# Kernel optimization log

Hardware: AMD Instinct MI355X
Metric: run time of the kernel (lower is better)

## Reference

```python
import jax, jax.numpy as jnp
import numpy as np


def _maxpool2x2(x):
    # x: [N, C, H, W] -> [N, C, H//2, W//2]
    return jax.lax.reduce_window(x, -jnp.inf, jax.lax.max,
                                 (1, 1, 2, 2), (1, 1, 2, 2), 'VALID')


def _head(a, W1, b1, W2, b2, W3, b3):
    # headModel: maxpool -> (adaptive avgpool to 7x7 is identity here) -> flatten -> classifier (eval mode)
    mp = _maxpool2x2(a)                      # [N, 512, 7, 7]
    flat = mp.reshape(mp.shape[0], -1)       # [N, 25088]
    h = jax.nn.relu(flat @ W1.T + b1)        # [N, 4096]
    h = jax.nn.relu(h @ W2.T + b2)           # [N, 4096]
    return h @ W3.T + b3                     # [N, 1000]


def setup_inputs() -> dict:
    key = jax.random.key(0)
    ks = jax.random.split(key, 7)
    C, HW, FC, NC = 512, 14, 4096, 1000
    acts = jax.random.uniform(ks[0], (1, C, HW, HW), dtype=jnp.float32)  # post-ReLU feature map
    s1 = 1.0 / np.sqrt(C * 7 * 7)
    s2 = 1.0 / np.sqrt(FC)
    return {
        'activations': acts,
        'W1': jax.random.normal(ks[1], (FC, C * 7 * 7), dtype=jnp.float32) * s1,
        'b1': jax.random.normal(ks[2], (FC,), dtype=jnp.float32) * 0.01,
        'W2': jax.random.normal(ks[3], (FC, FC), dtype=jnp.float32) * s2,
        'b2': jax.random.normal(ks[4], (FC,), dtype=jnp.float32) * 0.01,
        'W3': jax.random.normal(ks[5], (NC, FC), dtype=jnp.float32) * s2,
        'b3': jax.random.normal(ks[6], (NC,), dtype=jnp.float32) * 0.01,
        'ht': 224,
        'wt': 224,
    }


def reference(activations, W1, b1, W2, b2, W3, b3, ht, wt):
    C = activations.shape[1]
    logits = _head(activations, W1, b1, W2, b2, W3, b3)   # [1, 1000]
    img_class = jnp.argmax(logits[0])
    base = logits[0, img_class]

    # Batch all C channel ablations: abl[i] = activations with channel i zeroed.
    mask = (1.0 - jnp.eye(C, dtype=activations.dtype))[:, :, None, None]  # [C, C, 1, 1]
    abl = activations * mask                                              # [C, C, 14, 14]
    logits_new = _head(abl, W1, b1, W2, b2, W3, b3)                        # [C, 1000]
    alpha = (base - jnp.take(logits_new, img_class, axis=1)) / base        # [C]

    # fused = relu(sum_i alpha_i * bilinear_resize(act_i)); resize is linear,
    # so weight in activation space and do one resize (same math as the loop).
    weighted = jnp.einsum('c,chw->hw', alpha, activations[0])              # [14, 14]
    sal = jax.image.resize(weighted[None, None], (1, 1, ht, wt),
                           method='bilinear')[0, 0]                        # [ht, wt]
    fused = jax.nn.relu(sal)
    mn, mx = fused.min(), fused.max()
    denom = jnp.where(mx != mn, mx - mn, 1.0)
    fused = jnp.where(mx != mn, (fused - mn) / denom, fused)
    return fused, img_class
```

## Files before the change

### kernel.cpp

```cpp
#include <hip/hip_runtime.h>
#include <math.h>

#define CCH 512
#define F1 25088
#define FC 4096
#define NCLS 1000
#define OW 224
#define KSPLIT 8
#define KSL 512
#define PSTRIDE (CCH*FC)

#define WS_DT 0
#define WS_MP (WS_DT + FC*CCH)
#define WS_H1PRE (WS_MP + F1)
#define WS_H1 (WS_H1PRE + FC)
#define WS_H2 (WS_H1 + FC)
#define WS_H2PART (WS_H2 + FC)
#define WS_LOGITS (WS_H2PART + 8*FC)
#define WS_CLSBASE (WS_LOGITS + NCLS)
#define WS_ALPHA (WS_CLSBASE + 2)
#define WS_MINMAX (WS_ALPHA + CCH)
#define WS_LOGPART (WS_MINMAX + 2)
#define WS_A (WS_LOGPART + 64*CCH)
#define WS_PARTB (WS_A + CCH*FC/2)
#define WS_END (WS_PARTB + KSPLIT*CCH*FC/2)
#define WS_NEED_BYTES ((size_t)WS_END * 4)

typedef __attribute__((ext_vector_type(8))) short bfrag;
typedef __attribute__((ext_vector_type(4))) float f32x4;

static __device__ __forceinline__ unsigned short f2bf(float x) {
    unsigned u = __float_as_uint(x);
    unsigned r = 0x7FFFu + ((u >> 16) & 1u);
    return (unsigned short)((u + r) >> 16);
}

#define GLD16(g, l) __builtin_amdgcn_global_load_lds( \
    (const __attribute__((address_space(1))) void*)(g), \
    (__attribute__((address_space(3))) void*)(l), 16, 0, 0)

__global__ void k_maxpool(const float* __restrict__ act, float* __restrict__ ws) {
    int t = threadIdx.x;
    if (blockIdx.x == 0) {
        if (t == 0) ((int*)(ws + WS_MINMAX))[0] = 0x7F800000;
        if (t == 1) ((int*)(ws + WS_MINMAX))[1] = 0;
    }
    int idx = blockIdx.x * 256 + t;
    if (idx >= CCH * 49) return;
    int c = idx / 49, r = idx % 49, y = r / 7, x = r % 7;
    const float* a = act + c * 196 + (2 * y) * 14 + 2 * x;
    float m = fmaxf(fmaxf(a[0], a[1]), fmaxf(a[14], a[15]));
    ws[WS_MP + idx] = m;
}

__global__ __launch_bounds__(256) void k_phi7(const float* __restrict__ W1,
                                              const float* __restrict__ mp,
                                              const float* __restrict__ b1,
                                              float* __restrict__ Dt,
                                              float* __restrict__ h1pre,
                                              float* __restrict__ h1) {
    __shared__ float buf[12544];
    __shared__ float red[256];
    int j = blockIdx.x, t = threadIdx.x;
    const float4* wrow = (const float4*)(W1 + (size_t)j * F1);
    const float4* mrow = (const float4*)mp;
    float sh = 0.f;
    #pragma unroll
    for (int h = 0; h < 2; ++h) {
        const float4* src = wrow + h * 3136;
        const float4* msc = mrow + h * 3136;
        __syncthreads();
        #pragma unroll
        for (int b = 0; b < 2; ++b) {
            float4 w[6], m[6];
            #pragma unroll
            for (int e = 0; e < 6; ++e) {
                int n = t + 256 * (b * 6 + e);
                w[e] = src[n]; m[e] = msc[n];
            }
            #pragma unroll
            for (int e = 0; e < 6; ++e) {
                int n = t + 256 * (b * 6 + e);
                float4 p;
                p.x = w[e].x * m[e].x; p.y = w[e].y * m[e].y;
                p.z = w[e].z * m[e].z; p.w = w[e].w * m[e].w;
                *(float4*)&buf[n * 4] = p;
            }
        }
        if (t < 64) {
            int n = 3072 + t;
            float4 w = src[n], m = msc[n];
            float4 p;
            p.x = w.x * m.x; p.y = w.y * m.y; p.z = w.z * m.z; p.w = w.w * m.w;
            *(float4*)&buf[n * 4] = p;
        }
        __syncthreads();
        const float* bb = buf + t * 49;
        float s = 0.f;
        #pragma unroll
        for (int k = 0; k < 49; ++k) s += bb[k];
        Dt[(size_t)j * CCH + h * 256 + t] = s;
        sh += s;
    }
    red[t] = sh;
    __syncthreads();
    if (t < 128) red[t] += red[t + 128];
    __syncthreads();
    if (t < 64) {
        float v = red[t] + red[t + 64];
        for (int off = 32; off > 0; off >>= 1) v += __shfl_down(v, off, 64);
        if (t == 0) { float hv = b1[j] + v; h1pre[j] = hv; h1[j] = fmaxf(hv, 0.f); }
    }
}

template <bool RELU>
__global__ void k_gemv4096(const float* __restrict__ M, const float* __restrict__ v,
                           const float* __restrict__ bias, float* __restrict__ out) {
    int j = blockIdx.x, t = threadIdx.x;
    const float4* row = (const float4*)(M + (size_t)j * FC);
    const float4* vv = (const float4*)v;
    float s = 0.f;
    #pragma unroll
    for (int q = 0; q < 4; ++q) {
        int n = q * 256 + t;
        float4 w = row[n], x = vv[n];
        s += w.x * x.x + w.y * x.y + w.z * x.z + w.w * x.w;
    }
    __shared__ float red[256];
    red[t] = s; __syncthreads();
    if (t < 128) red[t] += red[t + 128]; __syncthreads();
    if (t < 64)  red[t] += red[t + 64];  __syncthreads();
    if (t < 64) {
        float x = red[t];
        for (int off = 32; off > 0; off >>= 1) x += __shfl_down(x, off, 64);
        if (t == 0) { float r2 = bias[j] + x; out[j] = RELU ? fmaxf(r2, 0.f) : r2; }
    }
}

__global__ void k_argmax(const float* __restrict__ logits, float* __restrict__ clsbase,
                         float* __restrict__ dout_cls) {
    int t = threadIdx.x;
    float best = -INFINITY; int bi = NCLS;
    for (int n = t; n < NCLS; n += 256) {
        float v = logits[n];
        if (v > best || (v == best && n < bi)) { best = v; bi = n; }
    }
    __shared__ float bv[256]; __shared__ int bidx[256];
    bv[t] = best; bidx[t] = bi; __syncthreads();
    for (int o = 128; o > 0; o >>= 1) {
        if (t < o) {
            float v2 = bv[t + o]; int i2 = bidx[t + o];
            if (v2 > bv[t] || (v2 == bv[t] && i2 < bidx[t])) { bv[t] = v2; bidx[t] = i2; }
        }
        __syncthreads();
    }
    if (t == 0) { clsbase[0] = (float)bidx[0]; clsbase[1] = bv[0]; *dout_cls = (float)bidx[0]; }
}

__global__ __launch_bounds__(256) void k_abuild(const float* __restrict__ Dt,
                                                const float* __restrict__ h1pre,
                                                unsigned short* __restrict__ A) {
    __shared__ unsigned short tile[64][72];
    int kt = blockIdx.x, it = blockIdx.y, t = threadIdx.x;
    int k0 = kt * 64, i0 = it * 64;
    #pragma unroll
    for (int q = 0; q < 16; ++q) {
        int kk = q * 4 + (t >> 6);
        int ii = t & 63;
        float v = fmaxf(h1pre[k0 + kk] - Dt[(size_t)(k0 + kk) * CCH + i0 + ii], 0.f);
        tile[kk][ii] = f2bf(v);
    }
    __syncthreads();
    #pragma unroll
    for (int q = 0; q < 4; ++q) {
        int c = q * 256 + t;
        int ii = c >> 4, kc = c & 15;
        ushort4 v;
        v.x = tile[kc * 4 + 0][ii]; v.y = tile[kc * 4 + 1][ii];
        v.z = tile[kc * 4 + 2][ii]; v.w = tile[kc * 4 + 3][ii];
        *(ushort4*)&A[(size_t)(i0 + ii) * FC + k0 + kc * 4] = v;
    }
}

__global__ __launch_bounds__(512) void k_mfma_v6(
    const unsigned short* __restrict__ A, const float* __restrict__ W2,
    const float* __restrict__ h1, unsigned short* __restrict__ partb,
    float* __restrict__ h2part) {
    __shared__ char As[2][32768];
    __shared__ char Bs[2][4096];
    __shared__ float h1s[KSL];
    int bid = blockIdx.x;
    int ks = bid & 7, nj = bid >> 3;
    int t = threadIdx.x;
    int wid = t >> 6, lane = t & 63, lr = lane & 15, lh = lane >> 4;
    int j0 = nj * 64;
    int kb = ks * KSL;

    h1s[t] = h1[kb + t];
    __syncthreads();

    int brow = t >> 3, bkc = t & 7;
    const float* wsrc = W2 + (size_t)(j0 + brow) * FC + kb + bkc * 4;
    int bsw = (brow & 3) ^ ((brow >> 2) & 1);
    int boff = (brow * 4 + ((bkc >> 1) ^ bsw)) * 16 + (bkc & 1) * 8;

    float hacc = 0.f;
    f32x4 acc[4][4];
    #pragma unroll
    for (int f = 0; f < 4; ++f)
        #pragma unroll
        for (int n = 0; n < 4; ++n) acc[f][n] = (f32x4){0.f, 0.f, 0.f, 0.f};

    #pragma unroll
    for (int r = 0; r < 4; ++r) {
        int c = t + 512 * r;
        int row = c >> 2, ch = c & 3;
        int sw = (row & 3) ^ ((row >> 2) & 1);
        GLD16(A + (size_t)row * FC + kb + ((ch ^ sw) * 8), As[0] + (size_t)c * 16);
    }
    {
        float4 w = *(const float4*)wsrc;
        hacc += w.x * h1s[bkc * 4 + 0] + w.y * h1s[bkc * 4 + 1]
              + w.z * h1s[bkc * 4 + 2] + w.w * h1s[bkc * 4 + 3];
        ushort4 pk;
        pk.x = f2bf(w.x); pk.y = f2bf(w.y); pk.z = f2bf(w.z); pk.w = f2bf(w.w);
        *(ushort4*)(Bs[0] + boff) = pk;
    }
    __syncthreads();

    int cur = 0;
    for (int kst = 0; kst + 32 < KSL; kst += 32) {
        int nxt = kst + 32;
        #pragma unroll
        for (int r = 0; r < 4; ++r) {
            int c = t + 512 * r;
            int row = c >> 2, ch = c & 3;
            int sw = (row & 3) ^ ((row >> 2) & 1);
            GLD16(A + (size_t)row * FC + kb + nxt + ((ch ^ sw) * 8),
                  As[cur ^ 1] + (size_t)c * 16);
        }
        float4 w = *(const float4*)(wsrc + nxt);
        {
            bfrag bfr[4];
            #pragma unroll
            for (int n = 0; n < 4; ++n) {
                int br = n * 16 + lr;
                int swb = (br & 3) ^ ((br >> 2) & 1);
                bfr[n] = *(const bfrag*)(Bs[cur] + (br * 4 + (lh ^ swb)) * 16);
            }
            #pragma unroll
            for (int f = 0; f < 4; ++f) {
                int ar = wid * 64 + f * 16 + lr;
                int swa = (ar & 3) ^ ((ar >> 2) & 1);
                bfrag av = *(const bfrag*)(As[cur] + (ar * 4 + (lh ^ swa)) * 16);
                #pragma unroll
                for (int n = 0; n < 4; ++n)
                    acc[f][n] = __builtin_amdgcn_mfma_f32_16x16x32_bf16(av, bfr[n], acc[f][n], 0, 0, 0);
            }
        }
        hacc += w.x * h1s[nxt + bkc * 4 + 0] + w.y * h1s[nxt + bkc * 4 + 1]
              + w.z * h1s[nxt + bkc * 4 + 2] + w.w * h1s[nxt + bkc * 4 + 3];
        {
            ushort4 pk;
            pk.x = f2bf(w.x); pk.y = f2bf(w.y); pk.z = f2bf(w.z); pk.w = f2bf(w.w);
            *(ushort4*)(Bs[cur ^ 1] + boff) = pk;
        }
        __syncthreads();
        cur ^= 1;
    }
    {
        bfrag bfr[4];
        #pragma unroll
        for (int n = 0; n < 4; ++n) {
            int br = n * 16 + lr;
            int swb = (br & 3) ^ ((br >> 2) & 1);
            bfr[n] = *(const bfrag*)(Bs[cur] + (br * 4 + (lh ^ swb)) * 16);
        }
        #pragma unroll
        for (int f = 0; f < 4; ++f) {
            int ar = wid * 64 + f * 16 + lr;
            int swa = (ar & 3) ^ ((ar >> 2) & 1);
            bfrag av = *(const bfrag*)(As[cur] + (ar * 4 + (lh ^ swa)) * 16);
            #pragma unroll
            for (int n = 0; n < 4; ++n)
                acc[f][n] = __builtin_amdgcn_mfma_f32_16x16x32_bf16(av, bfr[n], acc[f][n], 0, 0, 0);
        }
    }

    hacc += __shfl_down(hacc, 4, 8);
    hacc += __shfl_down(hacc, 2, 8);
    hacc += __shfl_down(hacc, 1, 8);
    if (bkc == 0) h2part[ks * FC + j0 + brow] = hacc;

    unsigned short* pb = partb + (size_t)ks * PSTRIDE;
    #pragma unroll
    for (int f = 0; f < 4; ++f) {
        int row0 = wid * 64 + f * 16 + lh * 4;
        #pragma unroll
        for (int rr = 0; rr < 4; ++rr)
            #pragma unroll
            for (int n = 0; n < 4; ++n)
                pb[(size_t)(row0 + rr) * FC + j0 + n * 16 + lr] = f2bf(acc[f][n][rr]);
    }
}

__global__ void k_h2sum(const float* __restrict__ h2part, const float* __restrict__ b2,
                        float* __restrict__ h2) {
    int j = blockIdx.x * 256 + threadIdx.x;
    if (j < FC) {
        float v = b2[j];
        #pragma unroll
        for (int p = 0; p < KSPLIT; ++p) v += h2part[p * FC + j];
        h2[j] = fmaxf(v, 0.f);
    }
}

__global__ __launch_bounds__(256) void k_alpha_b(
    const unsigned short* __restrict__ partb, const float* __restrict__ b2,
    const float* __restrict__ W3, const float* __restrict__ b3,
    const float* __restrict__ clsbase, float* __restrict__ alpha) {
    int i = blockIdx.x, t = threadIdx.x;
    int cls = (int)clsbase[0]; float base = clsbase[1];
    const float* w3r = W3 + (size_t)cls * FC;
    float s = 0.f;
    #pragma unroll
    for (int q = 0; q < 2; ++q) {
        int jj = (q * 256 + t) * 8;
        float acc8[8];
        #pragma unroll
        for (int e = 0; e < 8; ++e) acc8[e] = b2[jj + e];
        #pragma unroll
        for (int p = 0; p < KSPLIT; ++p) {
            uint4 pv = *(const uint4*)(partb + (size_t)p * PSTRIDE + (size_t)i * FC + jj);
            #pragma unroll
            for (int e = 0; e < 4; ++e) {
                unsigned a = ((const unsigned*)&pv)[e];
                acc8[e * 2]     += __uint_as_float(a << 16);
                acc8[e * 2 + 1] += __uint_as_float(a & 0xFFFF0000u);
            }
        }
        #pragma unroll
        for (int e = 0; e < 8; ++e) s += fmaxf(acc8[e], 0.f) * w3r[jj + e];
    }
    __shared__ float red[256];
    red[t] = s; __syncthreads();
    if (t < 128) red[t] += red[t + 128]; __syncthreads();
    if (t < 64)  red[t] += red[t + 64];  __syncthreads();
    if (t < 64) {
        float x = red[t];
        for (int off = 32; off > 0; off >>= 1) x += __shfl_down(x, off, 64);
        if (t == 0) alpha[i] = (base - (x + b3[cls])) / base;
    }
}

__global__ __launch_bounds__(256) void k_gemm_abl(
    const float* __restrict__ Dt, const float* __restrict__ h1pre,
    const float* __restrict__ W2, const float* __restrict__ b2,
    const float* __restrict__ W3, const float* __restrict__ clsbase,
    float* __restrict__ logit_part) {
    int mi = blockIdx.x, nj = blockIdx.y, t = threadIdx.x;
    int tx = t & 15, ty = t >> 4;
    int i0 = mi * 64, j0 = nj * 64;
    __shared__ float As2[16][64];
    __shared__ float Bs2[16][65];
    float acc[4][4] = {};
    for (int k0 = 0; k0 < FC; k0 += 16) {
        #pragma unroll
        for (int r = 0; r < 4; ++r) {
            int e = t + 256 * r; int kk = e >> 6, ii = e & 63;
            As2[kk][ii] = fmaxf(h1pre[k0 + kk] - Dt[(size_t)(k0 + kk) * CCH + i0 + ii], 0.f);
        }
        {
            int jj = t >> 2, kks = (t & 3) * 4;
            const float4 wv = *(const float4*)(W2 + (size_t)(j0 + jj) * FC + k0 + kks);
            Bs2[kks + 0][jj] = wv.x; Bs2[kks + 1][jj] = wv.y;
            Bs2[kks + 2][jj] = wv.z; Bs2[kks + 3][jj] = wv.w;
        }
        __syncthreads();
        #pragma unroll
        for (int kk = 0; kk < 16; ++kk) {
            float4 a4 = *(const float4*)&As2[kk][tx * 4];
            float av[4] = {a4.x, a4.y, a4.z, a4.w};
            float bv[4] = {Bs2[kk][ty * 4 + 0], Bs2[kk][ty * 4 + 1],
                           Bs2[kk][ty * 4 + 2], Bs2[kk][ty * 4 + 3]};
            #pragma unroll
            for (int a = 0; a < 4; ++a)
                #pragma unroll
                for (int bb = 0; bb < 4; ++bb)
                    acc[a][bb] = fmaf(av[a], bv[bb], acc[a][bb]);
        }
        __syncthreads();
    }
    int cls = (int)clsbase[0];
    const float* w3r = W3 + (size_t)cls * FC;
    float prt[4] = {0.f, 0.f, 0.f, 0.f};
    #pragma unroll
    for (int bb = 0; bb < 4; ++bb) {
        int j2 = j0 + ty * 4 + bb;
        float b2v = b2[j2], w3 = w3r[j2];
        #pragma unroll
        for (int a = 0; a < 4; ++a) prt[a] = fmaf(fmaxf(acc[a][bb] + b2v, 0.f), w3, prt[a]);
    }
    __shared__ float red2[16][68];
    #pragma unroll
    for (int a = 0; a < 4; ++a) red2[ty][tx * 4 + a] = prt[a];
    __syncthreads();
    if (t < 64) {
        float s = 0.f;
        #pragma unroll
        for (int q = 0; q < 16; ++q) s += red2[q][t];
        logit_part[nj * CCH + i0 + t] = s;
    }
}

__global__ void k_alpha_fb(const float* __restrict__ logit_part, const float* __restrict__ b3,
                           const float* __restrict__ clsbase, float* __restrict__ alpha) {
    int t = blockIdx.x * 256 + threadIdx.x;
    if (t >= CCH) return;
    int cls = (int)clsbase[0]; float base = clsbase[1];
    float s = 0.f;
    for (int q = 0; q < 64; ++q) s += logit_part[q * CCH + t];
    alpha[t] = (base - (s + b3[cls])) / base;
}

__global__ void k_resize2(const float* __restrict__ alpha, const float* __restrict__ act,
                          float* __restrict__ out, int* __restrict__ minmax) {
    __shared__ float sA[CCH];
    __shared__ float sW[196];
    int t = threadIdx.x;
    for (int i = t; i < CCH; i += 256) sA[i] = alpha[i];
    __syncthreads();
    if (t < 196) {
        float s = 0.f;
        for (int c = 0; c < CCH; ++c) s = fmaf(sA[c], act[c * 196 + t], s);
        sW[t] = s;
    }
    __syncthreads();
    int pix = blockIdx.x * 256 + t;
    int y = pix / OW, x = pix % OW;
    float uy = (y + 0.5f) * 0.0625f - 0.5f;
    float ux = (x + 0.5f) * 0.0625f - 0.5f;
    float y0f = floorf(uy), x0f = floorf(ux);
    float fy = uy - y0f, fx = ux - x0f;
    int y0 = (int)y0f, x0 = (int)x0f;
    int y0c = min(max(y0, 0), 13), y1c = min(max(y0 + 1, 0), 13);
    int x0c = min(max(x0, 0), 13), x1c = min(max(x0 + 1, 0), 13);
    float v00 = sW[y0c * 14 + x0c], v01 = sW[y0c * 14 + x1c];
    float v10 = sW[y1c * 14 + x0c], v11 = sW[y1c * 14 + x1c];
    float v0 = v00 + (v01 - v00) * fx;
    float v1 = v10 + (v11 - v10) * fx;
    float v = v0 + (v1 - v0) * fy;
    float f = fmaxf(v, 0.f);
    out[pix] = f;
    __shared__ float rmn[256], rmx[256];
    rmn[t] = f; rmx[t] = f; __syncthreads();
    for (int o = 128; o > 0; o >>= 1) {
        if (t < o) { rmn[t] = fminf(rmn[t], rmn[t + o]); rmx[t] = fmaxf(rmx[t], rmx[t + o]); }
        __syncthreads();
    }
    if (t == 0) {
        atomicMin(&minmax[0], __float_as_int(rmn[0]));
        atomicMax(&minmax[1], __float_as_int(rmx[0]));
    }
}

__global__ void k_norm(float* __restrict__ out, const int* __restrict__ minmax) {
    float mn = __int_as_float(minmax[0]);
    float mx = __int_as_float(minmax[1]);
    int pix = blockIdx.x * 256 + threadIdx.x;
    if (mx != mn) out[pix] = (out[pix] - mn) / (mx - mn);
}

extern "C" void kernel_launch(void* const* d_in, const int* in_sizes, int n_in,
                              void* d_out, int out_size, void* d_ws, size_t ws_size,
                              hipStream_t stream) {
    const float* act = (const float*)d_in[0];
    const float* W1  = (const float*)d_in[1];
    const float* b1  = (const float*)d_in[2];
    const float* W2  = (const float*)d_in[3];
    const float* b2  = (const float*)d_in[4];
    const float* W3  = (const float*)d_in[5];
    const float* b3  = (const float*)d_in[6];
    float* out = (float*)d_out;
    float* ws = (float*)d_ws;
    const bool fast = (ws_size >= WS_NEED_BYTES);

    k_maxpool<<<98, 256, 0, stream>>>(act, ws);
    k_phi7<<<4096, 256, 0, stream>>>(W1, ws + WS_MP, b1, ws + WS_DT,
                                     ws + WS_H1PRE, ws + WS_H1);
    if (fast) {
        k_abuild<<<dim3(64, 8), 256, 0, stream>>>(ws + WS_DT, ws + WS_H1PRE,
                                                  (unsigned short*)(ws + WS_A));
        k_mfma_v6<<<512, 512, 0, stream>>>(
            (const unsigned short*)(ws + WS_A), W2, ws + WS_H1,
            (unsigned short*)(ws + WS_PARTB), ws + WS_H2PART);
        k_h2sum<<<16, 256, 0, stream>>>(ws + WS_H2PART, b2, ws + WS_H2);
        k_gemv4096<false><<<1000, 256, 0, stream>>>(W3, ws + WS_H2, b3, ws + WS_LOGITS);
        k_argmax<<<1, 256, 0, stream>>>(ws + WS_LOGITS, ws + WS_CLSBASE, out + 50176);
        k_alpha_b<<<CCH, 256, 0, stream>>>((const unsigned short*)(ws + WS_PARTB), b2,
                                           W3, b3, ws + WS_CLSBASE, ws + WS_ALPHA);
    } else {
        k_gemv4096<true><<<4096, 256, 0, stream>>>(W2, ws + WS_H1, b2, ws + WS_H2);
        k_gemv4096<false><<<1000, 256, 0, stream>>>(W3, ws + WS_H2, b3, ws + WS_LOGITS);
        k_argmax<<<1, 256, 0, stream>>>(ws + WS_LOGITS, ws + WS_CLSBASE, out + 50176);
        k_gemm_abl<<<dim3(8, 64), 256, 0, stream>>>(ws + WS_DT, ws + WS_H1PRE, W2, b2,
                                                    W3, ws + WS_CLSBASE, ws + WS_LOGPART);
        k_alpha_fb<<<2, 256, 0, stream>>>(ws + WS_LOGPART, b3, ws + WS_CLSBASE,
                                          ws + WS_ALPHA);
    }
    k_resize2<<<196, 256, 0, stream>>>(ws + WS_ALPHA, act, out, (int*)(ws + WS_MINMAX));
    k_norm<<<196, 256, 0, stream>>>(out, (const int*)(ws + WS_MINMAX));
}
```

Before: 207.1 us.

## Fuse tail kernels using last-block atomic counters to cut launches

Merges the h2 sum, W3 GEMV and argmax into one kernel: every block recomputes h2 into shared memory, and the last block to finish, found with an atomic counter, does the argmax. It also merges the alpha computation, weighted sum, bilinear resize, relu and min/max normalization into a second kernel whose last block does the whole 224x224 epilogue. The aim is to remove several kernel launches and their serialization gaps. The cost is redundant h2 reduction in each of the 1000 blocks and a single-block epilogue over about 50k pixels, which runs serially on one CU.

Result: slower. 422.0 us (+103.8%).

```diff
diff --git a/kernel.cpp b/kernel.cpp
--- a/kernel.cpp
+++ b/kernel.cpp
@@ -20,7 +20,8 @@
 #define WS_CLSBASE (WS_LOGITS + NCLS)
 #define WS_ALPHA (WS_CLSBASE + 2)
 #define WS_MINMAX (WS_ALPHA + CCH)
-#define WS_LOGPART (WS_MINMAX + 2)
+#define WS_CNT (WS_MINMAX + 2)
+#define WS_LOGPART (WS_CNT + 2)
 #define WS_A (WS_LOGPART + 64*CCH)
 #define WS_PARTB (WS_A + CCH*FC/2)
 #define WS_END (WS_PARTB + KSPLIT*CCH*FC/2)
@@ -44,6 +45,8 @@
     if (blockIdx.x == 0) {
         if (t == 0) ((int*)(ws + WS_MINMAX))[0] = 0x7F800000;
         if (t == 1) ((int*)(ws + WS_MINMAX))[1] = 0;
+        if (t == 2) ((int*)(ws + WS_CNT))[0] = 0;
+        if (t == 3) ((int*)(ws + WS_CNT))[1] = 0;
     }
     int idx = blockIdx.x * 256 + t;
     if (idx >= CCH * 49) return;
@@ -111,50 +114,6 @@
         for (int off = 32; off > 0; off >>= 1) v += __shfl_down(v, off, 64);
         if (t == 0) { float hv = b1[j] + v; h1pre[j] = hv; h1[j] = fmaxf(hv, 0.f); }
     }
-}
-
-template <bool RELU>
-__global__ void k_gemv4096(const float* __restrict__ M, const float* __restrict__ v,
-                           const float* __restrict__ bias, float* __restrict__ out) {
-    int j = blockIdx.x, t = threadIdx.x;
-    const float4* row = (const float4*)(M + (size_t)j * FC);
-    const float4* vv = (const float4*)v;
-    float s = 0.f;
-    #pragma unroll
-    for (int q = 0; q < 4; ++q) {
-        int n = q * 256 + t;
-        float4 w = row[n], x = vv[n];
-        s += w.x * x.x + w.y * x.y + w.z * x.z + w.w * x.w;
-    }
-    __shared__ float red[256];
-    red[t] = s; __syncthreads();
-    if (t < 128) red[t] += red[t + 128]; __syncthreads();
-    if (t < 64)  red[t] += red[t + 64];  __syncthreads();
-    if (t < 64) {
-        float x = red[t];
-        for (int off = 32; off > 0; off >>= 1) x += __shfl_down(x, off, 64);
-        if (t == 0) { float r2 = bias[j] + x; out[j] = RELU ? fmaxf(r2, 0.f) : r2; }
-    }
-}
-
-__global__ void k_argmax(const float* __restrict__ logits, float* __restrict__ clsbase,
-                         float* __restrict__ dout_cls) {
-    int t = threadIdx.x;
-    float best = -INFINITY; int bi = NCLS;
-    for (int n = t; n < NCLS; n += 256) {
-        float v = logits[n];
-        if (v > best || (v == best && n < bi)) { best = v; bi = n; }
-    }
-    __shared__ float bv[256]; __shared__ int bidx[256];
-    bv[t] = best; bidx[t] = bi; __syncthreads();
-    for (int o = 128; o > 0; o >>= 1) {
-        if (t < o) {
-            float v2 = bv[t + o]; int i2 = bidx[t + o];
-            if (v2 > bv[t] || (v2 == bv[t] && i2 < bidx[t])) { bv[t] = v2; bidx[t] = i2; }
-        }
-        __syncthreads();
-    }
-    if (t == 0) { clsbase[0] = (float)bidx[0]; clsbase[1] = bv[0]; *dout_cls = (float)bidx[0]; }
 }
 
 __global__ __launch_bounds__(256) void k_abuild(const float* __restrict__ Dt,
@@ -304,23 +263,75 @@
     }
 }
 
-__global__ void k_h2sum(const float* __restrict__ h2part, const float* __restrict__ b2,
-                        float* __restrict__ h2) {
-    int j = blockIdx.x * 256 + threadIdx.x;
-    if (j < FC) {
-        float v = b2[j];
-        #pragma unroll
-        for (int p = 0; p < KSPLIT; ++p) v += h2part[p * FC + j];
-        h2[j] = fmaxf(v, 0.f);
-    }
-}
-
-__global__ __launch_bounds__(256) void k_alpha_b(
+__global__ __launch_bounds__(256) void k_tail1(
+    const float* __restrict__ h2part, const float* __restrict__ b2,
+    const float* __restrict__ W3, const float* __restrict__ b3,
+    float* __restrict__ ws, float* __restrict__ out, int* __restrict__ counter) {
+    __shared__ float h2s[FC];
+    __shared__ float red[256];
+    __shared__ int lastFlag;
+    int j = blockIdx.x, t = threadIdx.x;
+    #pragma unroll
+    for (int q = 0; q < 16; ++q) {
+        int jj = q * 256 + t;
+        float v = b2[jj];
+        #pragma unroll
+        for (int p = 0; p < KSPLIT; ++p) v += h2part[p * FC + jj];
+        h2s[jj] = fmaxf(v, 0.f);
+    }
+    __syncthreads();
+    const float4* row = (const float4*)(W3 + (size_t)j * FC);
+    const float4* hv = (const float4*)h2s;
+    float s = 0.f;
+    #pragma unroll
+    for (int q = 0; q < 4; ++q) {
+        int n = q * 256 + t;
+        float4 w = row[n], x = hv[n];
+        s += w.x * x.x + w.y * x.y + w.z * x.z + w.w * x.w;
+    }
+    red[t] = s; __syncthreads();
+    if (t < 128) red[t] += red[t + 128]; __syncthreads();
+    if (t < 64)  red[t] += red[t + 64];  __syncthreads();
+    if (t < 64) {
+        float x = red[t];
+        for (int off = 32; off > 0; off >>= 1) x += __shfl_down(x, off, 64);
+        if (t == 0) ws[WS_LOGITS + j] = x + b3[j];
+    }
+    __threadfence();
+    if (t == 0) lastFlag = (atomicAdd(counter, 1) == NCLS - 1);
+    __syncthreads();
+    if (!lastFlag) return;
+    __threadfence();
+    float best = -INFINITY; int bi = NCLS;
+    for (int n = t; n < NCLS; n += 256) {
+        float v = ws[WS_LOGITS + n];
+        if (v > best || (v == best && n < bi)) { best = v; bi = n; }
+    }
+    __shared__ float bv[256]; __shared__ int bidx[256];
+    bv[t] = best; bidx[t] = bi; __syncthreads();
+    for (int o = 128; o > 0; o >>= 1) {
+        if (t < o) {
+            float v2 = bv[t + o]; int i2 = bidx[t + o];
+            if (v2 > bv[t] || (v2 == bv[t] && i2 < bidx[t])) { bv[t] = v2; bidx[t] = i2; }
+        }
+        __syncthreads();
+    }
+    if (t == 0) {
+        ws[WS_CLSBASE] = (float)bidx[0];
+        ws[WS_CLSBASE + 1] = bv[0];
+        out[50176] = (float)bidx[0];
+    }
+}
+
+__global__ __launch_bounds__(256) void k_tail2(
     const unsigned short* __restrict__ partb, const float* __restrict__ b2,
     const float* __restrict__ W3, const float* __restrict__ b3,
-    const float* __restrict__ clsbase, float* __restrict__ alpha) {
+    const float* __restrict__ act, float* __restrict__ ws,
+    float* __restrict__ out, int* __restrict__ counter) {
+    __shared__ float red[256];
+    __shared__ int lastFlag;
     int i = blockIdx.x, t = threadIdx.x;
-    int cls = (int)clsbase[0]; float base = clsbase[1];
+    int cls = (int)ws[WS_CLSBASE]; float base = ws[WS_CLSBASE + 1];
     const float* w3r = W3 + (size_t)cls * FC;
     float s = 0.f;
     #pragma unroll
@@ -341,6 +352,75 @@
         }
         #pragma unroll
         for (int e = 0; e < 8; ++e) s += fmaxf(acc8[e], 0.f) * w3r[jj + e];
+    }
+    red[t] = s; __syncthreads();
+    if (t < 128) red[t] += red[t + 128]; __syncthreads();
+    if (t < 64)  red[t] += red[t + 64];  __syncthreads();
+    if (t < 64) {
+        float x = red[t];
+        for (int off = 32; off > 0; off >>= 1) x += __shfl_down(x, off, 64);
+        if (t == 0) ws[WS_ALPHA + i] = (base - (x + b3[cls])) / base;
+    }
+    __threadfence();
+    if (t == 0) lastFlag = (atomicAdd(counter, 1) == CCH - 1);
+    __syncthreads();
+    if (!lastFlag) return;
+    __threadfence();
+    __shared__ float sA[CCH];
+    __shared__ float sW[196];
+    for (int c = t; c < CCH; c += 256) sA[c] = ws[WS_ALPHA + c];
+    __syncthreads();
+    if (t < 196) {
+        float s2 = 0.f;
+        for (int c = 0; c < CCH; ++c) s2 = fmaf(sA[c], act[c * 196 + t], s2);
+        sW[t] = s2;
+    }
+    __syncthreads();
+    float mn = INFINITY, mx = -INFINITY;
+    for (int pix = t; pix < 50176; pix += 256) {
+        int y = pix / OW, x = pix % OW;
+        float uy = (y + 0.5f) * 0.0625f - 0.5f;
+        float ux = (x + 0.5f) * 0.0625f - 0.5f;
+        float y0f = floorf(uy), x0f = floorf(ux);
+        float fy = uy - y0f, fx = ux - x0f;
+        int y0 = (int)y0f, x0 = (int)x0f;
+        int y0c = min(max(y0, 0), 13), y1c = min(max(y0 + 1, 0), 13);
+        int x0c = min(max(x0, 0), 13), x1c = min(max(x0 + 1, 0), 13);
+        float v00 = sW[y0c * 14 + x0c], v01 = sW[y0c * 14 + x1c];
+        float v10 = sW[y1c * 14 + x0c], v11 = sW[y1c * 14 + x1c];
+        float v0 = v00 + (v01 - v00) * fx;
+        float v1 = v10 + (v11 - v10) * fx;
+        float v = v0 + (v1 - v0) * fy;
+        float f = fmaxf(v, 0.f);
+        out[pix] = f;
+        mn = fminf(mn, f); mx = fmaxf(mx, f);
+    }
+    __shared__ float rmn[256], rmx[256];
+    rmn[t] = mn; rmx[t] = mx; __syncthreads();
+    for (int o = 128; o > 0; o >>= 1) {
+        if (t < o) { rmn[t] = fminf(rmn[t], rmn[t + o]); rmx[t] = fmaxf(rmx[t], rmx[t + o]); }
+        __syncthreads();
+    }
+    mn = rmn[0]; mx = rmx[0];
+    if (mx != mn) {
+        float inv = 1.f / (mx - mn);
+        for (int pix = t; pix < 50176; pix += 256)
+            out[pix] = (out[pix] - mn) * inv;
+    }
+}
+
+template <bool RELU>
+__global__ void k_gemv4096(const float* __restrict__ M, const float* __restrict__ v,
+                           const float* __restrict__ bias, float* __restrict__ out) {
+    int j = blockIdx.x, t = threadIdx.x;
+    const float4* row = (const float4*)(M + (size_t)j * FC);
+    const float4* vv = (const float4*)v;
+    float s = 0.f;
+    #pragma unroll
+    for (int q = 0; q < 4; ++q) {
+        int n = q * 256 + t;
+        float4 w = row[n], x = vv[n];
+        s += w.x * x.x + w.y * x.y + w.z * x.z + w.w * x.w;
     }
     __shared__ float red[256];
     red[t] = s; __syncthreads();
@@ -349,8 +429,28 @@
     if (t < 64) {
         float x = red[t];
         for (int off = 32; off > 0; off >>= 1) x += __shfl_down(x, off, 64);
-        if (t == 0) alpha[i] = (base - (x + b3[cls])) / base;
-    }
+        if (t == 0) { float r2 = bias[j] + x; out[j] = RELU ? fmaxf(r2, 0.f) : r2; }
+    }
+}
+
+__global__ void k_argmax(const float* __restrict__ logits, float* __restrict__ clsbase,
+                         float* __restrict__ dout_cls) {
+    int t = threadIdx.x;
+    float best = -INFINITY; int bi = NCLS;
+    for (int n = t; n < NCLS; n += 256) {
+        float v = logits[n];
+        if (v > best || (v == best && n < bi)) { best = v; bi = n; }
+    }
+    __shared__ float bv[256]; __shared__ int bidx[256];
+    bv[t] = best; bidx[t] = bi; __syncthreads();
+    for (int o = 128; o > 0; o >>= 1) {
+        if (t < o) {
+            float v2 = bv[t + o]; int i2 = bidx[t + o];
+            if (v2 > bv[t] || (v2 == bv[t] && i2 < bidx[t])) { bv[t] = v2; bidx[t] = i2; }
+        }
+        __syncthreads();
+    }
+    if (t == 0) { clsbase[0] = (float)bidx[0]; clsbase[1] = bv[0]; *dout_cls = (float)bidx[0]; }
 }
 
 __global__ __launch_bounds__(256) void k_gemm_abl(
@@ -494,11 +594,11 @@
         k_mfma_v6<<<512, 512, 0, stream>>>(
             (const unsigned short*)(ws + WS_A), W2, ws + WS_H1,
             (unsigned short*)(ws + WS_PARTB), ws + WS_H2PART);
-        k_h2sum<<<16, 256, 0, stream>>>(ws + WS_H2PART, b2, ws + WS_H2);
-        k_gemv4096<false><<<1000, 256, 0, stream>>>(W3, ws + WS_H2, b3, ws + WS_LOGITS);
-        k_argmax<<<1, 256, 0, stream>>>(ws + WS_LOGITS, ws + WS_CLSBASE, out + 50176);
-        k_alpha_b<<<CCH, 256, 0, stream>>>((const unsigned short*)(ws + WS_PARTB), b2,
-                                           W3, b3, ws + WS_CLSBASE, ws + WS_ALPHA);
+        k_tail1<<<NCLS, 256, 0, stream>>>(ws + WS_H2PART, b2, W3, b3, ws, out,
+                                          (int*)(ws + WS_CNT));
+        k_tail2<<<CCH, 256, 0, stream>>>((const unsigned short*)(ws + WS_PARTB), b2,
+                                         W3, b3, act, ws, out,
+                                         (int*)(ws + WS_CNT) + 1);
     } else {
         k_gemv4096<true><<<4096, 256, 0, stream>>>(W2, ws + WS_H1, b2, ws + WS_H2);
         k_gemv4096<false><<<1000, 256, 0, stream>>>(W3, ws + WS_H2, b3, ws + WS_LOGITS);
@@ -507,7 +607,7 @@
                                                     W3, ws + WS_CLSBASE, ws + WS_LOGPART);
         k_alpha_fb<<<2, 256, 0, stream>>>(ws + WS_LOGPART, b3, ws + WS_CLSBASE,
                                           ws + WS_ALPHA);
-    }
-    k_resize2<<<196, 256, 0, stream>>>(ws + WS_ALPHA, act, out, (int*)(ws + WS_MINMAX));
-    k_norm<<<196, 256, 0, stream>>>(out, (const int*)(ws + WS_MINMAX));
-}
+        k_resize2<<<196, 256, 0, stream>>>(ws + WS_ALPHA, act, out, (int*)(ws + WS_MINMAX));
+        k_norm<<<196, 256, 0, stream>>>(out, (const int*)(ws + WS_MINMAX));
+    }
+}
```
